# Kernel tuning notes

Hardware: AMD Instinct MI355X
Metric: run time of the kernel (lower is better)

The kernel has to match this reference:

```python
import jax, jax.numpy as jnp
import numpy as np

E = 1024   # embedding_dim
H = 16     # heads
W = 1024   # lag / seq length
B = 4      # batch
D = E // H # head dim


def setup_inputs() -> dict:
    key = jax.random.key(0)
    ks = jax.random.split(key, 5)
    scale = E ** -0.5
    return {
        "x":   jax.random.normal(ks[0], (3, B, E, W), dtype=jnp.float32),
        "L_Q": jax.random.normal(ks[1], (E, E), dtype=jnp.float32) * scale,
        "L_K": jax.random.normal(ks[2], (E, E), dtype=jnp.float32) * scale,
        "L_V": jax.random.normal(ks[3], (E, E), dtype=jnp.float32) * scale,
        "M":   jax.random.normal(ks[4], (E, E), dtype=jnp.float32) * (1.0 / (2 * E)) ** 0.5,
        "b":   jnp.zeros((E, 1), dtype=jnp.float32),
    }


def reference(x, L_Q, L_K, L_V, M, b):
    # x: [3, B, E, W] channels-first; x[0]=K input, x[1]=Q input, x[2]=V input
    K = jnp.einsum('ef,bfw->bew', L_K, x[0])
    Q = jnp.einsum('ef,bfw->bew', L_Q, x[1])
    V = jnp.einsum('ef,bfw->bew', L_V, x[2])
    # reshape to [B, H, D, W]
    Kv = K.reshape(B, H, D, W)
    Qv = Q.reshape(B, H, D, W)
    Vv = V.reshape(B, H, D, W)
    # scores[b,h,q,k] = Q_v^T @ K_v
    scores = jnp.einsum('bhdq,bhdk->bhqk', Qv, Kv)
    # causal mask: -inf for q > k (strictly lower triangle), added BEFORE softmax
    q_idx = jnp.arange(W)[:, None]
    k_idx = jnp.arange(W)[None, :]
    mask = jnp.where(q_idx > k_idx, -jnp.inf, 0.0).astype(scores.dtype)
    scores = scores + mask
    # NON-STANDARD: softmax over the QUERY axis (dim=-2), then scale
    attn = jax.nn.softmax(scores, axis=-2) / (E ** 0.5)
    # V_v @ scores: [B,H,D,W] @ [B,H,W,W] -> [B,H,D,W]
    out = jnp.einsum('bhdq,bhqk->bhdk', Vv, attn).reshape(B, E, W)
    # dense: M @ out + b (dropout identity at inference)
    return jnp.einsum('oe,bew->bow', M, out) + b
```

## Files before the change

kernel.cpp:

```cpp
#include <hip/hip_runtime.h>
#include <stdint.h>
#include <math.h>

#define E_DIM 1024
#define W_DIM 1024
#define EW 1048576L

typedef _Float16 h16;
typedef __attribute__((ext_vector_type(8))) _Float16 h8;
typedef __attribute__((ext_vector_type(4))) float f4;

__device__ __forceinline__ void async_copy16(h16* lds, const h16* g) {
    __builtin_amdgcn_global_load_lds(
        (const __attribute__((address_space(1))) void*)g,
        (__attribute__((address_space(3))) void*)lds, 16, 0, 0);
}

__global__ __launch_bounds__(256) void prep(
    const float* __restrict__ x, const float* __restrict__ LK,
    const float* __restrict__ LQ, const float* __restrict__ LV,
    const float* __restrict__ Mw, h16* __restrict__ xt, h16* __restrict__ wh)
{
    __shared__ float Ts[64][65];
    const int z = blockIdx.z;
    const int t = threadIdx.x;
    if (z < 12) {
        const float* src = x + (long)z * EW;
        h16* dst = xt + (long)z * EW;
        const int e0 = blockIdx.y * 64, w0 = blockIdx.x * 64;
        const int r = t >> 4, c4 = (t & 15) * 4;
        #pragma unroll
        for (int p = 0; p < 4; ++p) {
            float4 v = *reinterpret_cast<const float4*>(src + (long)(e0 + r + p * 16) * W_DIM + w0 + c4);
            Ts[c4 + 0][r + p * 16] = v.x;
            Ts[c4 + 1][r + p * 16] = v.y;
            Ts[c4 + 2][r + p * 16] = v.z;
            Ts[c4 + 3][r + p * 16] = v.w;
        }
        __syncthreads();
        #pragma unroll
        for (int p = 0; p < 4; ++p) {
            int wr = r + p * 16;
            union { h16 h[4]; uint2 u; } o;
            o.h[0] = (h16)Ts[wr][c4 + 0];
            o.h[1] = (h16)Ts[wr][c4 + 1];
            o.h[2] = (h16)Ts[wr][c4 + 2];
            o.h[3] = (h16)Ts[wr][c4 + 3];
            *reinterpret_cast<uint2*>(dst + (long)(w0 + wr) * E_DIM + e0 + c4) = o.u;
        }
    } else {
        const float* srcs[4] = {LK, LQ, LV, Mw};
        const float* s = srcs[z - 12];
        h16* o = wh + (long)(z - 12) * EW;
        long base = ((long)(blockIdx.y * 16 + blockIdx.x)) * 1024 + t;
        #pragma unroll
        for (int k = 0; k < 4; ++k) {
            long i = base + k * 256;
            float4 v = reinterpret_cast<const float4*>(s)[i];
            union { h16 h[4]; uint2 u; } u;
            u.h[0] = (h16)v.x; u.h[1] = (h16)v.y; u.h[2] = (h16)v.z; u.h[3] = (h16)v.w;
            reinterpret_cast<uint2*>(o)[i] = u.u;
        }
    }
}

__global__ __launch_bounds__(256) void gemm_proj3(
    const h16* __restrict__ xh, const h16* __restrict__ Wts,
    h16* __restrict__ KQV)
{
    __shared__ h16 As[128 * 32];
    __shared__ h16 Bs[128 * 32];

    const int t = threadIdx.x;
    const int wave = t >> 6, lane = t & 63;
    const int quad = lane >> 4, l16 = lane & 15;
    const int m0 = blockIdx.y * 128, n0 = blockIdx.x * 128;
    const int wm = (wave >> 1) * 64, wn = (wave & 1) * 64;

    const int proj = blockIdx.z >> 2, bz = blockIdx.z & 3;
    const h16 *A, *Bt; h16* C;
    if (proj == 0)      { A = xh + bz * EW;       Bt = Wts;          C = KQV + bz * EW; }
    else if (proj == 1) { A = xh + (4 + bz) * EW; Bt = Wts + EW;     C = KQV + (4 + bz) * EW; }
    else                { A = Wts + 2 * EW;       Bt = xh + (8 + bz) * EW; C = KQV + (8 + bz) * EW; }

    const int sr = t >> 2;
    const int sg = (t & 3) * 8;

    f4 acc[4][4] = {};

    for (int k0 = 0; k0 < 1024; k0 += 32) {
        __syncthreads();
        async_copy16(As + sr * 32 + sg,        A  + (long)(m0 + sr) * E_DIM + k0 + sg);
        async_copy16(As + (sr + 64) * 32 + sg, A  + (long)(m0 + sr + 64) * E_DIM + k0 + sg);
        async_copy16(Bs + sr * 32 + sg,        Bt + (long)(n0 + sr) * E_DIM + k0 + sg);
        async_copy16(Bs + (sr + 64) * 32 + sg, Bt + (long)(n0 + sr + 64) * E_DIM + k0 + sg);
        __syncthreads();

        h8 av[4], bv[4];
        #pragma unroll
        for (int i = 0; i < 4; ++i) {
            av[i] = *reinterpret_cast<const h8*>(As + (wm + i * 16 + l16) * 32 + quad * 8);
            bv[i] = *reinterpret_cast<const h8*>(Bs + (wn + i * 16 + l16) * 32 + quad * 8);
        }
        #pragma unroll
        for (int mt = 0; mt < 4; ++mt)
            #pragma unroll
            for (int nt = 0; nt < 4; ++nt)
                acc[mt][nt] = __builtin_amdgcn_mfma_f32_16x16x32_f16(av[mt], bv[nt], acc[mt][nt], 0, 0, 0);
    }

    #pragma unroll
    for (int mt = 0; mt < 4; ++mt)
        #pragma unroll
        for (int i = 0; i < 4; ++i) {
            int m = m0 + wm + mt * 16 + quad * 4 + i;
            #pragma unroll
            for (int nt = 0; nt < 4; ++nt)
                C[(long)m * W_DIM + n0 + wn + nt * 16 + l16] = (h16)acc[mt][nt][i];
        }
}

__global__ __launch_bounds__(256) void gemm_out(
    const h16* __restrict__ A, const h16* __restrict__ Bt,
    float* __restrict__ C, const float* __restrict__ bias)
{
    __shared__ h16 As[2][64 * 32];
    __shared__ h16 Bs[2][128 * 32];

    const int t = threadIdx.x;
    const int wave = t >> 6, lane = t & 63;
    const int quad = lane >> 4, l16 = lane & 15;
    const int m0 = blockIdx.y * 64, n0 = blockIdx.x * 128;
    const int wm = (wave >> 1) * 32, wn = (wave & 1) * 64;

    f4 acc[2][4] = {};

    const int ga_r = t >> 2, ga_c = (t & 3) * 8;

    {
        async_copy16(&As[0][t * 8], A + (long)(m0 + ga_r) * E_DIM + ga_c);
        #pragma unroll
        for (int j = 0; j < 2; ++j) {
            int g = j * 256 + t;
            async_copy16(&Bs[0][g * 8], Bt + (long)(n0 + (g >> 2)) * E_DIM + (g & 3) * 8);
        }
    }

    for (int it = 0; it < 32; ++it) {
        __syncthreads();
        if (it + 1 < 32) {
            int nb = (it + 1) & 1, k0 = (it + 1) * 32;
            async_copy16(&As[nb][t * 8], A + (long)(m0 + ga_r) * E_DIM + k0 + ga_c);
            #pragma unroll
            for (int j = 0; j < 2; ++j) {
                int g = j * 256 + t;
                async_copy16(&Bs[nb][g * 8], Bt + (long)(n0 + (g >> 2)) * E_DIM + k0 + (g & 3) * 8);
            }
        }
        const h16* as = As[it & 1];
        const h16* bs = Bs[it & 1];
        h8 av[2], bv[4];
        #pragma unroll
        for (int mt = 0; mt < 2; ++mt)
            av[mt] = *reinterpret_cast<const h8*>(as + (wm + mt * 16 + l16) * 32 + quad * 8);
        #pragma unroll
        for (int nt = 0; nt < 4; ++nt)
            bv[nt] = *reinterpret_cast<const h8*>(bs + (wn + nt * 16 + l16) * 32 + quad * 8);
        #pragma unroll
        for (int mt = 0; mt < 2; ++mt)
            #pragma unroll
            for (int nt = 0; nt < 4; ++nt)
                acc[mt][nt] = __builtin_amdgcn_mfma_f32_16x16x32_f16(av[mt], bv[nt], acc[mt][nt], 0, 0, 0);
    }

    #pragma unroll
    for (int mt = 0; mt < 2; ++mt)
        #pragma unroll
        for (int i = 0; i < 4; ++i) {
            int m = m0 + wm + mt * 16 + quad * 4 + i;
            float bv_ = bias ? bias[m] : 0.f;
            #pragma unroll
            for (int nt = 0; nt < 4; ++nt) {
                int n = n0 + wn + nt * 16 + l16;
                C[(long)(n >> 10) * EW + (long)m * W_DIM + (n & 1023)] = acc[mt][nt][i] + bv_;
            }
        }
}

__global__ __launch_bounds__(256) void attn_mfma(
    const h16* __restrict__ Kt, const h16* __restrict__ Qt,
    const h16* __restrict__ V, h16* __restrict__ AoT)
{
    __shared__ h16 Qs[2][64 * 64];
    __shared__ h16 Vs[2][64 * 64];
    __shared__ h16 Ps[4][16 * 72];

    const int t = threadIdx.x, wave = t >> 6, lane = t & 63;
    const int quad = lane >> 4, l16 = lane & 15;
    const int b = blockIdx.y >> 4, h = blockIdx.y & 15;
    const int kt = 15 - blockIdx.x;
    const int k0 = kt * 64;
    const int kw = wave * 16;

    const h16* Ktb = Kt + (long)b * EW + h * 64;
    const h16* Qtb = Qt + (long)b * EW + h * 64;
    const h16* Vb  = V  + (long)b * EW + (long)(h * 64) * W_DIM;

    h8 av0 = *reinterpret_cast<const h8*>(Ktb + (long)(k0 + kw + l16) * E_DIM + quad * 8);
    h8 av1 = *reinterpret_cast<const h8*>(Ktb + (long)(k0 + kw + l16) * E_DIM + 32 + quad * 8);

    const int swz0 = ((quad) ^ (l16 & 7)) * 8;
    const int swz1 = ((4 + quad) ^ (l16 & 7)) * 8;

    float mrow[4], al[4];
    #pragma unroll
    for (int i = 0; i < 4; ++i) mrow[i] = -1e30f;
    f4 O[4] = {};
    f4 Lacc = {};
    h8 ones;
    #pragma unroll
    for (int j = 0; j < 8; ++j) ones[j] = (h16)1.0f;

    #pragma unroll
    for (int j = 0; j < 2; ++j) {
        int g = j * 256 + t, row = g >> 3, cg = (g & 7) ^ (row & 7);
        async_copy16(&Qs[0][g * 8], Qtb + (long)row * E_DIM + cg * 8);
        async_copy16(&Vs[0][g * 8], Vb + (long)row * W_DIM + cg * 8);
    }

    for (int it = 0; it <= kt; ++it) {
        const int q0 = it * 64;
        __syncthreads();
        if (it < kt) {
            int nb = (it + 1) & 1, q1 = q0 + 64;
            #pragma unroll
            for (int j = 0; j < 2; ++j) {
                int g = j * 256 + t, row = g >> 3, cg = (g & 7) ^ (row & 7);
                async_copy16(&Qs[nb][g * 8], Qtb + (long)(q1 + row) * E_DIM + cg * 8);
                async_copy16(&Vs[nb][g * 8], Vb + (long)row * W_DIM + q1 + cg * 8);
            }
        }
        const h16* qs = Qs[it & 1];
        const h16* vs = Vs[it & 1];

        f4 S[4] = {};
        #pragma unroll
        for (int nt = 0; nt < 4; ++nt) {
            int rb = (nt * 16 + l16) * 64;
            h8 b0 = *reinterpret_cast<const h8*>(qs + rb + swz0);
            h8 b1 = *reinterpret_cast<const h8*>(qs + rb + swz1);
            S[nt] = __builtin_amdgcn_mfma_f32_16x16x32_f16(av0, b0, S[nt], 0, 0, 0);
            S[nt] = __builtin_amdgcn_mfma_f32_16x16x32_f16(av1, b1, S[nt], 0, 0, 0);
        }

        if (it == kt) {
            #pragma unroll
            for (int nt = 0; nt < 4; ++nt)
                #pragma unroll
                for (int i = 0; i < 4; ++i)
                    if (q0 + nt * 16 + l16 > k0 + kw + quad * 4 + i) S[nt][i] = -1e30f;
        }

        #pragma unroll
        for (int i = 0; i < 4; ++i) {
            float mx = fmaxf(fmaxf(S[0][i], S[1][i]), fmaxf(S[2][i], S[3][i]));
            mx = fmaxf(mx, __shfl_xor(mx, 1));
            mx = fmaxf(mx, __shfl_xor(mx, 2));
            mx = fmaxf(mx, __shfl_xor(mx, 4));
            mx = fmaxf(mx, __shfl_xor(mx, 8));
            float nm = fmaxf(mrow[i], mx);
            al[i] = __expf(mrow[i] - nm);
            mrow[i] = nm;
        }
        #pragma unroll
        for (int nt = 0; nt < 4; ++nt)
            #pragma unroll
            for (int i = 0; i < 4; ++i)
                S[nt][i] = __expf(S[nt][i] - mrow[i]);
        #pragma unroll
        for (int i = 0; i < 4; ++i) {
            Lacc[i] *= al[i];
            #pragma unroll
            for (int dt = 0; dt < 4; ++dt) O[dt][i] *= al[i];
        }

        #pragma unroll
        for (int nt = 0; nt < 4; ++nt)
            #pragma unroll
            for (int i = 0; i < 4; ++i)
                Ps[wave][(quad * 4 + i) * 72 + nt * 16 + l16] = (h16)S[nt][i];
        asm volatile("" ::: "memory");

        #pragma unroll
        for (int c = 0; c < 2; ++c) {
            h8 pa = *reinterpret_cast<const h8*>(&Ps[wave][l16 * 72 + c * 32 + quad * 8]);
            Lacc = __builtin_amdgcn_mfma_f32_16x16x32_f16(pa, ones, Lacc, 0, 0, 0);
            int sw = c ? swz1 : swz0;
            #pragma unroll
            for (int dt = 0; dt < 4; ++dt) {
                h8 vv = *reinterpret_cast<const h8*>(vs + (dt * 16 + l16) * 64 + sw);
                O[dt] = __builtin_amdgcn_mfma_f32_16x16x32_f16(pa, vv, O[dt], 0, 0, 0);
            }
        }
    }

    #pragma unroll
    for (int dt = 0; dt < 4; ++dt)
        #pragma unroll
        for (int i = 0; i < 4; ++i)
            AoT[(long)b * EW + (long)(k0 + kw + quad * 4 + i) * E_DIM + h * 64 + dt * 16 + l16] =
                (h16)(O[dt][i] / Lacc[i] * 0.03125f);
}

extern "C" void kernel_launch(void* const* d_in, const int* in_sizes, int n_in,
                              void* d_out, int out_size, void* d_ws, size_t ws_size,
                              hipStream_t stream)
{
    const float* x  = (const float*)d_in[0];
    const float* LQ = (const float*)d_in[1];
    const float* LK = (const float*)d_in[2];
    const float* LV = (const float*)d_in[3];
    const float* Mw = (const float*)d_in[4];
    const float* bb = (const float*)d_in[5];
    float* out = (float*)d_out;
    h16* ws = (h16*)d_ws;

    h16* xh  = ws;
    h16* LKh = ws + 12 * EW;
    h16* Mh  = ws + 15 * EW;
    h16* Kp  = ws + 16 * EW;
    h16* Qp  = ws + 20 * EW;
    h16* Vp  = ws + 24 * EW;
    h16* Ao  = ws + 28 * EW;

    dim3 blk(256);
    prep<<<dim3(16, 16, 16), blk, 0, stream>>>(x, LK, LQ, LV, Mw, xh, LKh);
    gemm_proj3<<<dim3(8, 8, 12), blk, 0, stream>>>(xh, LKh, Kp);
    attn_mfma<<<dim3(16, 64), blk, 0, stream>>>(Kp, Qp, Vp, Ao);
    gemm_out<<<dim3(32, 16), blk, 0, stream>>>(Mh, Ao, out, bb);
}
```

Baseline: 222.6 us.

## Double-buffer projection GEMM and restructure attention to per-wave direct loads

New measurement: 284.6 us. +27.8%, slower.

```diff
diff --git a/kernel.cpp b/kernel.cpp
--- a/kernel.cpp
+++ b/kernel.cpp
@@ -68,8 +68,8 @@
     const h16* __restrict__ xh, const h16* __restrict__ Wts,
     h16* __restrict__ KQV)
 {
-    __shared__ h16 As[128 * 32];
-    __shared__ h16 Bs[128 * 32];
+    __shared__ h16 As[2][128 * 32];
+    __shared__ h16 Bs[2][128 * 32];
 
     const int t = threadIdx.x;
     const int wave = t >> 6, lane = t & 63;
@@ -88,19 +88,28 @@
 
     f4 acc[4][4] = {};
 
-    for (int k0 = 0; k0 < 1024; k0 += 32) {
+    async_copy16(&As[0][sr * 32 + sg],        A  + (long)(m0 + sr) * E_DIM + sg);
+    async_copy16(&As[0][(sr + 64) * 32 + sg], A  + (long)(m0 + sr + 64) * E_DIM + sg);
+    async_copy16(&Bs[0][sr * 32 + sg],        Bt + (long)(n0 + sr) * E_DIM + sg);
+    async_copy16(&Bs[0][(sr + 64) * 32 + sg], Bt + (long)(n0 + sr + 64) * E_DIM + sg);
+
+    for (int it = 0; it < 32; ++it) {
         __syncthreads();
-        async_copy16(As + sr * 32 + sg,        A  + (long)(m0 + sr) * E_DIM + k0 + sg);
-        async_copy16(As + (sr + 64) * 32 + sg, A  + (long)(m0 + sr + 64) * E_DIM + k0 + sg);
-        async_copy16(Bs + sr * 32 + sg,        Bt + (long)(n0 + sr) * E_DIM + k0 + sg);
-        async_copy16(Bs + (sr + 64) * 32 + sg, Bt + (long)(n0 + sr + 64) * E_DIM + k0 + sg);
-        __syncthreads();
+        if (it + 1 < 32) {
+            int nb = (it + 1) & 1, k0 = (it + 1) * 32;
+            async_copy16(&As[nb][sr * 32 + sg],        A  + (long)(m0 + sr) * E_DIM + k0 + sg);
+            async_copy16(&As[nb][(sr + 64) * 32 + sg], A  + (long)(m0 + sr + 64) * E_DIM + k0 + sg);
+            async_copy16(&Bs[nb][sr * 32 + sg],        Bt + (long)(n0 + sr) * E_DIM + k0 + sg);
+            async_copy16(&Bs[nb][(sr + 64) * 32 + sg], Bt + (long)(n0 + sr + 64) * E_DIM + k0 + sg);
+        }
+        const h16* as = As[it & 1];
+        const h16* bs = Bs[it & 1];
 
         h8 av[4], bv[4];
         #pragma unroll
         for (int i = 0; i < 4; ++i) {
-            av[i] = *reinterpret_cast<const h8*>(As + (wm + i * 16 + l16) * 32 + quad * 8);
-            bv[i] = *reinterpret_cast<const h8*>(Bs + (wn + i * 16 + l16) * 32 + quad * 8);
+            av[i] = *reinterpret_cast<const h8*>(as + (wm + i * 16 + l16) * 32 + quad * 8);
+            bv[i] = *reinterpret_cast<const h8*>(bs + (wn + i * 16 + l16) * 32 + quad * 8);
         }
         #pragma unroll
         for (int mt = 0; mt < 4; ++mt)
@@ -137,13 +146,11 @@
 
     const int ga_r = t >> 2, ga_c = (t & 3) * 8;
 
-    {
-        async_copy16(&As[0][t * 8], A + (long)(m0 + ga_r) * E_DIM + ga_c);
-        #pragma unroll
-        for (int j = 0; j < 2; ++j) {
-            int g = j * 256 + t;
-            async_copy16(&Bs[0][g * 8], Bt + (long)(n0 + (g >> 2)) * E_DIM + (g & 3) * 8);
-        }
+    async_copy16(&As[0][t * 8], A + (long)(m0 + ga_r) * E_DIM + ga_c);
+    #pragma unroll
+    for (int j = 0; j < 2; ++j) {
+        int g = j * 256 + t;
+        async_copy16(&Bs[0][g * 8], Bt + (long)(n0 + (g >> 2)) * E_DIM + (g & 3) * 8);
     }
 
     for (int it = 0; it < 32; ++it) {
@@ -191,125 +198,114 @@
     const h16* __restrict__ Kt, const h16* __restrict__ Qt,
     const h16* __restrict__ V, h16* __restrict__ AoT)
 {
-    __shared__ h16 Qs[2][64 * 64];
-    __shared__ h16 Vs[2][64 * 64];
-    __shared__ h16 Ps[4][16 * 72];
+    __shared__ h16 Ps[4][16 * 136];
 
     const int t = threadIdx.x, wave = t >> 6, lane = t & 63;
     const int quad = lane >> 4, l16 = lane & 15;
     const int b = blockIdx.y >> 4, h = blockIdx.y & 15;
     const int kt = 15 - blockIdx.x;
-    const int k0 = kt * 64;
-    const int kw = wave * 16;
+    const int kbase = kt * 64 + wave * 16;
+    const int kcol = kbase + l16;
 
     const h16* Ktb = Kt + (long)b * EW + h * 64;
     const h16* Qtb = Qt + (long)b * EW + h * 64;
     const h16* Vb  = V  + (long)b * EW + (long)(h * 64) * W_DIM;
-
-    h8 av0 = *reinterpret_cast<const h8*>(Ktb + (long)(k0 + kw + l16) * E_DIM + quad * 8);
-    h8 av1 = *reinterpret_cast<const h8*>(Ktb + (long)(k0 + kw + l16) * E_DIM + 32 + quad * 8);
-
-    const int swz0 = ((quad) ^ (l16 & 7)) * 8;
-    const int swz1 = ((4 + quad) ^ (l16 & 7)) * 8;
-
-    float mrow[4], al[4];
-    #pragma unroll
-    for (int i = 0; i < 4; ++i) mrow[i] = -1e30f;
+    h16* Pw = &Ps[wave][0];
+
+    h8 kb0 = *reinterpret_cast<const h8*>(Ktb + (long)kcol * E_DIM + quad * 8);
+    h8 kb1 = *reinterpret_cast<const h8*>(Ktb + (long)kcol * E_DIM + 32 + quad * 8);
+
+    float mrow = -1e30f, lsum = 0.f;
     f4 O[4] = {};
-    f4 Lacc = {};
-    h8 ones;
-    #pragma unroll
-    for (int j = 0; j < 8; ++j) ones[j] = (h16)1.0f;
-
-    #pragma unroll
-    for (int j = 0; j < 2; ++j) {
-        int g = j * 256 + t, row = g >> 3, cg = (g & 7) ^ (row & 7);
-        async_copy16(&Qs[0][g * 8], Qtb + (long)row * E_DIM + cg * 8);
-        async_copy16(&Vs[0][g * 8], Vb + (long)row * W_DIM + cg * 8);
-    }
-
-    for (int it = 0; it <= kt; ++it) {
-        const int q0 = it * 64;
-        __syncthreads();
-        if (it < kt) {
-            int nb = (it + 1) & 1, q1 = q0 + 64;
-            #pragma unroll
-            for (int j = 0; j < 2; ++j) {
-                int g = j * 256 + t, row = g >> 3, cg = (g & 7) ^ (row & 7);
-                async_copy16(&Qs[nb][g * 8], Qtb + (long)(q1 + row) * E_DIM + cg * 8);
-                async_copy16(&Vs[nb][g * 8], Vb + (long)row * W_DIM + q1 + cg * 8);
-            }
-        }
-        const h16* qs = Qs[it & 1];
-        const h16* vs = Vs[it & 1];
-
-        f4 S[4] = {};
-        #pragma unroll
-        for (int nt = 0; nt < 4; ++nt) {
-            int rb = (nt * 16 + l16) * 64;
-            h8 b0 = *reinterpret_cast<const h8*>(qs + rb + swz0);
-            h8 b1 = *reinterpret_cast<const h8*>(qs + rb + swz1);
-            S[nt] = __builtin_amdgcn_mfma_f32_16x16x32_f16(av0, b0, S[nt], 0, 0, 0);
-            S[nt] = __builtin_amdgcn_mfma_f32_16x16x32_f16(av1, b1, S[nt], 0, 0, 0);
-        }
-
-        if (it == kt) {
-            #pragma unroll
-            for (int nt = 0; nt < 4; ++nt)
+
+    const int trips = (kbase + 15) / 128 + 1;
+
+    for (int it = 0; it < trips; ++it) {
+        const int q0 = it * 128;
+
+        f4 S[8];
+        #pragma unroll
+        for (int nt = 0; nt < 8; ++nt) {
+            const h16* qrow = Qtb + (long)(q0 + nt * 16 + l16) * E_DIM;
+            h8 qa0 = *reinterpret_cast<const h8*>(qrow + quad * 8);
+            h8 qa1 = *reinterpret_cast<const h8*>(qrow + 32 + quad * 8);
+            f4 s = {};
+            s = __builtin_amdgcn_mfma_f32_16x16x32_f16(qa0, kb0, s, 0, 0, 0);
+            s = __builtin_amdgcn_mfma_f32_16x16x32_f16(qa1, kb1, s, 0, 0, 0);
+            S[nt] = s;
+        }
+
+        if (it == trips - 1) {
+            #pragma unroll
+            for (int nt = 0; nt < 8; ++nt)
                 #pragma unroll
                 for (int i = 0; i < 4; ++i)
-                    if (q0 + nt * 16 + l16 > k0 + kw + quad * 4 + i) S[nt][i] = -1e30f;
-        }
-
-        #pragma unroll
-        for (int i = 0; i < 4; ++i) {
-            float mx = fmaxf(fmaxf(S[0][i], S[1][i]), fmaxf(S[2][i], S[3][i]));
-            mx = fmaxf(mx, __shfl_xor(mx, 1));
-            mx = fmaxf(mx, __shfl_xor(mx, 2));
-            mx = fmaxf(mx, __shfl_xor(mx, 4));
-            mx = fmaxf(mx, __shfl_xor(mx, 8));
-            float nm = fmaxf(mrow[i], mx);
-            al[i] = __expf(mrow[i] - nm);
-            mrow[i] = nm;
-        }
-        #pragma unroll
-        for (int nt = 0; nt < 4; ++nt)
-            #pragma unroll
-            for (int i = 0; i < 4; ++i)
-                S[nt][i] = __expf(S[nt][i] - mrow[i]);
-        #pragma unroll
-        for (int i = 0; i < 4; ++i) {
-            Lacc[i] *= al[i];
-            #pragma unroll
-            for (int dt = 0; dt < 4; ++dt) O[dt][i] *= al[i];
-        }
-
-        #pragma unroll
-        for (int nt = 0; nt < 4; ++nt)
-            #pragma unroll
-            for (int i = 0; i < 4; ++i)
-                Ps[wave][(quad * 4 + i) * 72 + nt * 16 + l16] = (h16)S[nt][i];
+                    if (q0 + nt * 16 + quad * 4 + i > kcol) S[nt][i] = -1e30f;
+        }
+
+        float mx = -1e30f;
+        #pragma unroll
+        for (int nt = 0; nt < 8; ++nt)
+            #pragma unroll
+            for (int i = 0; i < 4; ++i) mx = fmaxf(mx, S[nt][i]);
+        mx = fmaxf(mx, __shfl_xor(mx, 16));
+        mx = fmaxf(mx, __shfl_xor(mx, 32));
+        float nm = fmaxf(mrow, mx);
+        float al = __expf(mrow - nm);
+        mrow = nm;
+
+        float ts = 0.f;
+        #pragma unroll
+        for (int nt = 0; nt < 8; ++nt)
+            #pragma unroll
+            for (int i = 0; i < 4; ++i) {
+                float p = __expf(S[nt][i] - nm);
+                S[nt][i] = p;
+                ts += p;
+            }
+        ts += __shfl_xor(ts, 16);
+        ts += __shfl_xor(ts, 32);
+        lsum = lsum * al + ts;
+        #pragma unroll
+        for (int dt = 0; dt < 4; ++dt)
+            #pragma unroll
+            for (int i = 0; i < 4; ++i) O[dt][i] *= al;
+
+        #pragma unroll
+        for (int nt = 0; nt < 8; ++nt) {
+            union { h16 hh[4]; uint2 u2; } p;
+            p.hh[0] = (h16)S[nt][0]; p.hh[1] = (h16)S[nt][1];
+            p.hh[2] = (h16)S[nt][2]; p.hh[3] = (h16)S[nt][3];
+            *reinterpret_cast<uint2*>(Pw + l16 * 136 + nt * 16 + quad * 4) = p.u2;
+        }
         asm volatile("" ::: "memory");
 
         #pragma unroll
-        for (int c = 0; c < 2; ++c) {
-            h8 pa = *reinterpret_cast<const h8*>(&Ps[wave][l16 * 72 + c * 32 + quad * 8]);
-            Lacc = __builtin_amdgcn_mfma_f32_16x16x32_f16(pa, ones, Lacc, 0, 0, 0);
-            int sw = c ? swz1 : swz0;
+        for (int c = 0; c < 4; ++c) {
+            h8 pb = *reinterpret_cast<const h8*>(Pw + l16 * 136 + c * 32 + quad * 8);
             #pragma unroll
             for (int dt = 0; dt < 4; ++dt) {
-                h8 vv = *reinterpret_cast<const h8*>(vs + (dt * 16 + l16) * 64 + sw);
-                O[dt] = __builtin_amdgcn_mfma_f32_16x16x32_f16(pa, vv, O[dt], 0, 0, 0);
+                h8 va = *reinterpret_cast<const h8*>(Vb + (long)(dt * 16 + l16) * W_DIM + q0 + c * 32 + quad * 8);
+                O[dt] = __builtin_amdgcn_mfma_f32_16x16x32_f16(va, pb, O[dt], 0, 0, 0);
             }
         }
     }
 
-    #pragma unroll
-    for (int dt = 0; dt < 4; ++dt)
-        #pragma unroll
-        for (int i = 0; i < 4; ++i)
-            AoT[(long)b * EW + (long)(k0 + kw + quad * 4 + i) * E_DIM + h * 64 + dt * 16 + l16] =
-                (h16)(O[dt][i] / Lacc[i] * 0.03125f);
+    float inv = 0.03125f / lsum;
+    #pragma unroll
+    for (int dt = 0; dt < 4; ++dt) {
+        union { h16 hh[4]; uint2 u2; } p;
+        #pragma unroll
+        for (int i = 0; i < 4; ++i) p.hh[i] = (h16)(O[dt][i] * inv);
+        *reinterpret_cast<uint2*>(Pw + l16 * 136 + dt * 16 + quad * 4) = p.u2;
+    }
+    asm volatile("" ::: "memory");
+    #pragma unroll
+    for (int j = 0; j < 2; ++j) {
+        uint4 vv = *reinterpret_cast<const uint4*>(Pw + l16 * 136 + quad * 16 + j * 8);
+        *reinterpret_cast<uint4*>(AoT + (long)b * EW + (long)(kbase + l16) * E_DIM
+                                  + h * 64 + quad * 16 + j * 8) = vv;
+    }
 }
 
 extern "C" void kernel_launch(void* const* d_in, const int* in_sizes, int n_in,
```
